# Kernel optimization log

Measured on AMD Instinct MI355X. Metric: run time of the kernel, lower is better.

The kernel has to match this reference:

```python
import jax, jax.numpy as jnp
import numpy as np

M = 8192          # tokens
DIM = 2048        # per-stream width; K = 4*DIM
S = 4             # fixed stream count (Stream4 kernels)
N = 32            # fixed GEMM output width
SINKHORN_ITERS = 20


def setup_inputs() -> dict:
    key = jax.random.key(0)
    k1, k2 = jax.random.split(key)
    X = jax.random.normal(k1, (M, S * DIM), dtype=jnp.float32)
    # scale W so H = X @ W is O(1): keeps sigmoid/exp/sinkhorn numerically sane
    W = jax.random.normal(k2, (S * DIM, N), dtype=jnp.float32) / np.float32(np.sqrt(S * DIM))
    # module init: beta = zeros(24), alpha = ones(3), concatenated
    alpha_beta = jnp.concatenate([jnp.zeros(24, jnp.float32), jnp.ones(3, jnp.float32)])
    return {"X": X, "W": W, "alpha_beta": alpha_beta}


def _sinkhorn(P, iters=SINKHORN_ITERS):
    # doubly-stochastic normalization of [M, S, S] matrices
    for _ in range(iters):
        P = P / jnp.sum(P, axis=-1, keepdims=True)  # row normalize
        P = P / jnp.sum(P, axis=-2, keepdims=True)  # col normalize
    return P


def reference(X, W, alpha_beta):
    Mm, K = X.shape
    d = K // S
    # skinny GEMM producing the mixing logits (fused w/ SplitK in the kernel)
    H = X @ W                                   # [M, 32]
    b_res, b_pre, b_pos = alpha_beta[0:16], alpha_beta[16:20], alpha_beta[20:24]
    a_res, a_pre, a_pos = alpha_beta[24], alpha_beta[25], alpha_beta[26]
    H_pre = a_pre * jax.nn.sigmoid(H[:, 16:20]) + b_pre          # [M, 4]
    H_pos = a_pos * jax.nn.sigmoid(H[:, 20:24]) + b_pos          # [M, 4]
    H_res = (a_res * H[:, 0:16] + b_res).reshape(Mm, S, S)       # [M, 4, 4]
    H_res = _sinkhorn(jnp.exp(H_res))                            # doubly stochastic
    # view X as 4 streams of width d
    Xs = X.reshape(Mm, S, d)                                     # [M, 4, d]
    # ApplyPreTransform: collapse streams with H_pre weights
    Y = jnp.einsum('ms,msd->md', H_pre, Xs)                      # [M, d]
    # ApplyResidual: per-token 4x4 stream mix + broadcast of pre-transformed feature
    O = jnp.einsum('msi,mid->msd', H_res, Xs) + H_pos[:, :, None] * Y[:, None, :]
    return O.reshape(Mm, K)
```

## Files before the change

### kernel.cpp

```cpp
#include <hip/hip_runtime.h>
#include <math.h>
#include <stdint.h>

#define K_DIM 8192
#define D_DIM 2048
#define M_ROWS 8192
#define N_W 32
#define NC 24
#define KSPLIT 8
#define ROWS 16
#define THR 256
#define ITERS 8

typedef short bf16x8 __attribute__((ext_vector_type(8)));
typedef float f32x4 __attribute__((ext_vector_type(4)));
union U32x4 { uint32_t u[4]; bf16x8 v; };

#define WFI(ks, tile) (((ks) * 2 + (tile)) * 64)

__global__ __launch_bounds__(256) void mhc_prepack_kernel(
    const float* __restrict__ W, unsigned short* __restrict__ wfrag,
    float* __restrict__ Hsum)
{
    const int idx = blockIdx.x * 256 + threadIdx.x;
    const int k = idx >> 5, n = idx & 31;
    const float w = W[(size_t)k * N_W + n];
    const uint32_t u = __float_as_uint(w);
    const uint32_t r = u + 0x7FFFu + ((u >> 16) & 1u);

    const int ks = k >> 5, kk = k & 31;
    const int lane = ((kk >> 3) << 4) | (n & 15);
    const int e = kk & 7;
    const int tile = n >> 4;
    wfrag[((size_t)WFI(ks, tile) + lane) * 8 + e] = (unsigned short)(r >> 16);

    if (idx < M_ROWS * NC) Hsum[idx] = 0.f;
}

__global__ __launch_bounds__(THR) void mhc_gemm_kernel(
    const float* __restrict__ X, const unsigned short* __restrict__ wfrag,
    float* __restrict__ Hsum)
{
    __shared__ __align__(16) float4 Xl[4][2][128];
    const int t = threadIdx.x;
    const int l = t & 63;
    const int wv = t >> 6;
    const int rowbase = blockIdx.x * ROWS;
    const int ks0 = blockIdx.y * 32 + wv * ITERS;

    const float4* __restrict__ Xg = reinterpret_cast<const float4*>(X);
    const bf16x8* __restrict__ wf = reinterpret_cast<const bf16x8*>(wfrag);

    const int lr = l >> 3;
    const int lu = l & 7;
    const int arow = l & 15;
    const int au = (l >> 4) * 2;

    f32x4 c0 = {0.f, 0.f, 0.f, 0.f};
    f32x4 c1 = {0.f, 0.f, 0.f, 0.f};
    float4 pa, pb;
    bf16x8 b0n, b1n;

    pa = Xg[(size_t)(rowbase + lr) * (K_DIM / 4) + ks0 * 8 + lu];
    pb = Xg[(size_t)(rowbase + 8 + lr) * (K_DIM / 4) + ks0 * 8 + lu];
    b0n = wf[WFI(ks0, 0) + l];
    b1n = wf[WFI(ks0, 1) + l];
    Xl[wv][0][lr * 8 + (lu ^ lr)] = pa;
    Xl[wv][0][(8 + lr) * 8 + (lu ^ lr)] = pb;

#pragma unroll
    for (int i = 0; i < ITERS; ++i) {
        const bf16x8 b0 = b0n, b1 = b1n;
        if (i + 1 < ITERS) {
            const int ks = ks0 + i + 1;
            pa = Xg[(size_t)(rowbase + lr) * (K_DIM / 4) + ks * 8 + lu];
            pb = Xg[(size_t)(rowbase + 8 + lr) * (K_DIM / 4) + ks * 8 + lu];
            b0n = wf[WFI(ks, 0) + l];
            b1n = wf[WFI(ks, 1) + l];
        }

        const float4 xa = Xl[wv][i & 1][arow * 8 + (au ^ (arow & 7))];
        const float4 xb = Xl[wv][i & 1][arow * 8 + ((au + 1) ^ (arow & 7))];
        float xs[8];
        xs[0] = xa.x; xs[1] = xa.y; xs[2] = xa.z; xs[3] = xa.w;
        xs[4] = xb.x; xs[5] = xb.y; xs[6] = xb.z; xs[7] = xb.w;

        U32x4 ah, al;
#pragma unroll
        for (int p = 0; p < 4; ++p) {
            const uint32_t u0 = __float_as_uint(xs[2 * p]);
            const uint32_t u1 = __float_as_uint(xs[2 * p + 1]);
            const float h0 = __uint_as_float(u0 & 0xFFFF0000u);
            const float h1 = __uint_as_float(u1 & 0xFFFF0000u);
            const uint32_t r0 = __float_as_uint(xs[2 * p] - h0);
            const uint32_t r1 = __float_as_uint(xs[2 * p + 1] - h1);
            ah.u[p] = (u1 & 0xFFFF0000u) | (u0 >> 16);
            al.u[p] = (r1 & 0xFFFF0000u) | (r0 >> 16);
        }

        c0 = __builtin_amdgcn_mfma_f32_16x16x32_bf16(ah.v, b0, c0, 0, 0, 0);
        c0 = __builtin_amdgcn_mfma_f32_16x16x32_bf16(al.v, b0, c0, 0, 0, 0);
        c1 = __builtin_amdgcn_mfma_f32_16x16x32_bf16(ah.v, b1, c1, 0, 0, 0);
        c1 = __builtin_amdgcn_mfma_f32_16x16x32_bf16(al.v, b1, c1, 0, 0, 0);

        if (i + 1 < ITERS) {
            Xl[wv][(i + 1) & 1][lr * 8 + (lu ^ lr)] = pa;
            Xl[wv][(i + 1) & 1][(8 + lr) * 8 + (lu ^ lr)] = pb;
        }
    }

    const int drow = rowbase + ((l >> 4) << 2);
    const int col = l & 15;
#pragma unroll
    for (int r = 0; r < 4; ++r)
        atomicAdd(&Hsum[(size_t)(drow + r) * NC + col], c0[r]);
    if (col < 8) {
#pragma unroll
        for (int r = 0; r < 4; ++r)
            atomicAdd(&Hsum[(size_t)(drow + r) * NC + 16 + col], c1[r]);
    }
}

__global__ __launch_bounds__(256) void mhc_apply_kernel(
    const float* __restrict__ X, const float* __restrict__ Hsum,
    const float* __restrict__ ab, float* __restrict__ out)
{
    __shared__ float pbuf[NC];
    const int row = blockIdx.x;
    const int t = threadIdx.x;

    if (t < 64) {
        const int lane = t;
        const float pl = (lane < NC) ? Hsum[(size_t)row * NC + lane] : 0.f;
        const float bias  = (lane < NC) ? ab[lane] : 0.f;
        const float scale = ab[(lane < 16) ? 24 : ((lane < 20) ? 25 : 26)];

        float vout;
        if (lane < 16) {
            vout = __expf(fmaf(scale, pl, bias));
        } else {
            vout = fmaf(scale, 1.f / (1.f + __expf(-pl)), bias);
        }

        float p = vout;
        for (int it = 0; it < 20; ++it) {
            float rs = p + __shfl_xor(p, 1);
            rs += __shfl_xor(rs, 2);
            p = p / rs;
            float cs = p + __shfl_xor(p, 4);
            cs += __shfl_xor(cs, 8);
            p = p / cs;
        }
        if (lane < NC) pbuf[lane] = (lane < 16) ? p : vout;
    }
    __syncthreads();

    float hres[4][4], hpre[4], hpos[4];
#pragma unroll
    for (int i = 0; i < 16; ++i) hres[i >> 2][i & 3] = pbuf[i];
#pragma unroll
    for (int i = 0; i < 4; ++i) hpre[i] = pbuf[16 + i];
#pragma unroll
    for (int i = 0; i < 4; ++i) hpos[i] = pbuf[20 + i];

    const float4* __restrict__ Xr =
        reinterpret_cast<const float4*>(X + (size_t)row * K_DIM);
    float4* __restrict__ Or = reinterpret_cast<float4*>(out + (size_t)row * K_DIM);

#pragma unroll
    for (int q = 0; q < 2; ++q) {
        const int pos = t + q * 256;
        float4 xq[4];
#pragma unroll
        for (int i = 0; i < 4; ++i) xq[i] = Xr[i * (D_DIM / 4) + pos];

        float y[4];
#pragma unroll
        for (int e = 0; e < 4; ++e) {
            float s = 0.f;
#pragma unroll
            for (int i = 0; i < 4; ++i)
                s = fmaf(hpre[i], reinterpret_cast<const float*>(&xq[i])[e], s);
            y[e] = s;
        }

#pragma unroll
        for (int s = 0; s < 4; ++s) {
            float4 o;
            float* oe = reinterpret_cast<float*>(&o);
#pragma unroll
            for (int e = 0; e < 4; ++e) {
                float v = hpos[s] * y[e];
#pragma unroll
                for (int i = 0; i < 4; ++i)
                    v = fmaf(hres[s][i], reinterpret_cast<const float*>(&xq[i])[e], v);
                oe[e] = v;
            }
            Or[s * (D_DIM / 4) + pos] = o;
        }
    }
}

extern "C" void kernel_launch(void* const* d_in, const int* in_sizes, int n_in,
                              void* d_out, int out_size, void* d_ws, size_t ws_size,
                              hipStream_t stream) {
    const float* X  = (const float*)d_in[0];
    const float* W  = (const float*)d_in[1];
    const float* ab = (const float*)d_in[2];
    float* out = (float*)d_out;
    unsigned short* wfrag = (unsigned short*)d_ws;
    float* Hsum = (float*)((char*)d_ws + 524288);

    mhc_prepack_kernel<<<(K_DIM * N_W) / 256, 256, 0, stream>>>(W, wfrag, Hsum);
    dim3 g1(M_ROWS / ROWS, KSPLIT);
    mhc_gemm_kernel<<<g1, THR, 0, stream>>>(X, wfrag, Hsum);
    mhc_apply_kernel<<<M_ROWS, 256, 0, stream>>>(X, Hsum, ab, out);
}
```

Measured before the change: 173.1 us.

## Replace atomic split-K reduction with partial buffers and register-prefetched direct loads

```diff
diff --git a/kernel.cpp b/kernel.cpp
--- a/kernel.cpp
+++ b/kernel.cpp
@@ -7,10 +7,12 @@
 #define M_ROWS 8192
 #define N_W 32
 #define NC 24
-#define KSPLIT 8
+#define KSPLIT 16
+#define KSB 16
 #define ROWS 16
-#define THR 256
-#define ITERS 8
+#define THR 64
+#define DX 4
+#define DB 2
 
 typedef short bf16x8 __attribute__((ext_vector_type(8)));
 typedef float f32x4 __attribute__((ext_vector_type(4)));
@@ -19,8 +21,7 @@
 #define WFI(ks, tile) (((ks) * 2 + (tile)) * 64)
 
 __global__ __launch_bounds__(256) void mhc_prepack_kernel(
-    const float* __restrict__ W, unsigned short* __restrict__ wfrag,
-    float* __restrict__ Hsum)
+    const float* __restrict__ W, unsigned short* __restrict__ wfrag)
 {
     const int idx = blockIdx.x * 256 + threadIdx.x;
     const int k = idx >> 5, n = idx & 31;
@@ -33,54 +34,55 @@
     const int e = kk & 7;
     const int tile = n >> 4;
     wfrag[((size_t)WFI(ks, tile) + lane) * 8 + e] = (unsigned short)(r >> 16);
-
-    if (idx < M_ROWS * NC) Hsum[idx] = 0.f;
 }
 
 __global__ __launch_bounds__(THR) void mhc_gemm_kernel(
     const float* __restrict__ X, const unsigned short* __restrict__ wfrag,
-    float* __restrict__ Hsum)
+    float* __restrict__ part)
 {
-    __shared__ __align__(16) float4 Xl[4][2][128];
-    const int t = threadIdx.x;
-    const int l = t & 63;
-    const int wv = t >> 6;
+    const int l = threadIdx.x;
     const int rowbase = blockIdx.x * ROWS;
-    const int ks0 = blockIdx.y * 32 + wv * ITERS;
+    const int ks0 = blockIdx.y * KSB;
 
     const float4* __restrict__ Xg = reinterpret_cast<const float4*>(X);
     const bf16x8* __restrict__ wf = reinterpret_cast<const bf16x8*>(wfrag);
 
-    const int lr = l >> 3;
-    const int lu = l & 7;
-    const int arow = l & 15;
-    const int au = (l >> 4) * 2;
+    const int arow = rowbase + (l & 15);
+    const size_t xbase = (size_t)arow * (K_DIM / 4) + ((l >> 4) << 1);
 
     f32x4 c0 = {0.f, 0.f, 0.f, 0.f};
     f32x4 c1 = {0.f, 0.f, 0.f, 0.f};
-    float4 pa, pb;
-    bf16x8 b0n, b1n;
-
-    pa = Xg[(size_t)(rowbase + lr) * (K_DIM / 4) + ks0 * 8 + lu];
-    pb = Xg[(size_t)(rowbase + 8 + lr) * (K_DIM / 4) + ks0 * 8 + lu];
-    b0n = wf[WFI(ks0, 0) + l];
-    b1n = wf[WFI(ks0, 1) + l];
-    Xl[wv][0][lr * 8 + (lu ^ lr)] = pa;
-    Xl[wv][0][(8 + lr) * 8 + (lu ^ lr)] = pb;
-
-#pragma unroll
-    for (int i = 0; i < ITERS; ++i) {
-        const bf16x8 b0 = b0n, b1 = b1n;
-        if (i + 1 < ITERS) {
-            const int ks = ks0 + i + 1;
-            pa = Xg[(size_t)(rowbase + lr) * (K_DIM / 4) + ks * 8 + lu];
-            pb = Xg[(size_t)(rowbase + 8 + lr) * (K_DIM / 4) + ks * 8 + lu];
-            b0n = wf[WFI(ks, 0) + l];
-            b1n = wf[WFI(ks, 1) + l];
-        }
-
-        const float4 xa = Xl[wv][i & 1][arow * 8 + (au ^ (arow & 7))];
-        const float4 xb = Xl[wv][i & 1][arow * 8 + ((au + 1) ^ (arow & 7))];
+
+    float4 px[DX][2];
+    bf16x8 pb[DB][2];
+
+#pragma unroll
+    for (int i = 0; i < DX; ++i) {
+        px[i][0] = Xg[xbase + (size_t)(ks0 + i) * 8];
+        px[i][1] = Xg[xbase + (size_t)(ks0 + i) * 8 + 1];
+    }
+#pragma unroll
+    for (int i = 0; i < DB; ++i) {
+        pb[i][0] = wf[WFI(ks0 + i, 0) + l];
+        pb[i][1] = wf[WFI(ks0 + i, 1) + l];
+    }
+
+#pragma unroll
+    for (int i = 0; i < KSB; ++i) {
+        const float4 xa = px[i & (DX - 1)][0];
+        const float4 xb = px[i & (DX - 1)][1];
+        const bf16x8 b0 = pb[i & (DB - 1)][0];
+        const bf16x8 b1 = pb[i & (DB - 1)][1];
+
+        if (i + DX < KSB) {
+            px[i & (DX - 1)][0] = Xg[xbase + (size_t)(ks0 + i + DX) * 8];
+            px[i & (DX - 1)][1] = Xg[xbase + (size_t)(ks0 + i + DX) * 8 + 1];
+        }
+        if (i + DB < KSB) {
+            pb[i & (DB - 1)][0] = wf[WFI(ks0 + i + DB, 0) + l];
+            pb[i & (DB - 1)][1] = wf[WFI(ks0 + i + DB, 1) + l];
+        }
+
         float xs[8];
         xs[0] = xa.x; xs[1] = xa.y; xs[2] = xa.z; xs[3] = xa.w;
         xs[4] = xb.x; xs[5] = xb.y; xs[6] = xb.z; xs[7] = xb.w;
@@ -102,27 +104,23 @@
         c0 = __builtin_amdgcn_mfma_f32_16x16x32_bf16(al.v, b0, c0, 0, 0, 0);
         c1 = __builtin_amdgcn_mfma_f32_16x16x32_bf16(ah.v, b1, c1, 0, 0, 0);
         c1 = __builtin_amdgcn_mfma_f32_16x16x32_bf16(al.v, b1, c1, 0, 0, 0);
-
-        if (i + 1 < ITERS) {
-            Xl[wv][(i + 1) & 1][lr * 8 + (lu ^ lr)] = pa;
-            Xl[wv][(i + 1) & 1][(8 + lr) * 8 + (lu ^ lr)] = pb;
-        }
-    }
-
-    const int drow = rowbase + ((l >> 4) << 2);
+    }
+
+    float* prow = part + ((size_t)blockIdx.y * M_ROWS + rowbase) * NC;
+    const int drow0 = (l >> 4) << 2;
     const int col = l & 15;
 #pragma unroll
     for (int r = 0; r < 4; ++r)
-        atomicAdd(&Hsum[(size_t)(drow + r) * NC + col], c0[r]);
+        prow[(drow0 + r) * NC + col] = c0[r];
     if (col < 8) {
 #pragma unroll
         for (int r = 0; r < 4; ++r)
-            atomicAdd(&Hsum[(size_t)(drow + r) * NC + 16 + col], c1[r]);
+            prow[(drow0 + r) * NC + 16 + col] = c1[r];
     }
 }
 
 __global__ __launch_bounds__(256) void mhc_apply_kernel(
-    const float* __restrict__ X, const float* __restrict__ Hsum,
+    const float* __restrict__ X, const float* __restrict__ part,
     const float* __restrict__ ab, float* __restrict__ out)
 {
     __shared__ float pbuf[NC];
@@ -131,7 +129,12 @@
 
     if (t < 64) {
         const int lane = t;
-        const float pl = (lane < NC) ? Hsum[(size_t)row * NC + lane] : 0.f;
+        float pl = 0.f;
+        if (lane < NC) {
+#pragma unroll
+            for (int j = 0; j < KSPLIT; ++j)
+                pl += part[((size_t)j * M_ROWS + row) * NC + lane];
+        }
         const float bias  = (lane < NC) ? ab[lane] : 0.f;
         const float scale = ab[(lane < 16) ? 24 : ((lane < 20) ? 25 : 26)];
 
@@ -209,10 +212,10 @@
     const float* ab = (const float*)d_in[2];
     float* out = (float*)d_out;
     unsigned short* wfrag = (unsigned short*)d_ws;
-    float* Hsum = (float*)((char*)d_ws + 524288);
-
-    mhc_prepack_kernel<<<(K_DIM * N_W) / 256, 256, 0, stream>>>(W, wfrag, Hsum);
+    float* part = (float*)((char*)d_ws + 524288);
+
+    mhc_prepack_kernel<<<(K_DIM * N_W) / 256, 256, 0, stream>>>(W, wfrag);
     dim3 g1(M_ROWS / ROWS, KSPLIT);
-    mhc_gemm_kernel<<<g1, THR, 0, stream>>>(X, wfrag, Hsum);
-    mhc_apply_kernel<<<M_ROWS, 256, 0, stream>>>(X, Hsum, ab, out);
-}
+    mhc_gemm_kernel<<<g1, THR, 0, stream>>>(X, wfrag, part);
+    mhc_apply_kernel<<<M_ROWS, 256, 0, stream>>>(X, part, ab, out);
+}
```

Result: slower. 176.9 us (+2.2%).
